# Kernel tuning notes

Measured on AMD Instinct MI355X. Metric: run time of the kernel, lower is better.

The kernel has to match this reference:

```python
import jax, jax.numpy as jnp
import numpy as np

EPS = 1e-12  # F.normalize eps
WIN_SIZE = 200
WIN_STEP = 30  # eval mode (training uses 10)
N_WIN = 30     # 31 windows from length-1100 axis, last one dropped


def setup_inputs() -> dict:
    key = jax.random.key(0)
    ks = jax.random.split(key, 6)
    dim, K, out_dim = 128, 64, 256
    N, H, W = 8, 16, 900
    s = 1.0 / np.sqrt(dim)
    return {
        "x": jax.random.normal(ks[0], (N, dim, H, W), dtype=jnp.float32),
        "cluster_centers": jax.random.uniform(ks[1], (K, dim), dtype=jnp.float32),
        "conv_w": jax.random.normal(ks[2], (K, dim), dtype=jnp.float32) * s,
        "conv_b": jax.random.normal(ks[3], (K,), dtype=jnp.float32) * s,
        "mlp_w": jax.random.normal(ks[4], (out_dim, K * dim), dtype=jnp.float32) * s,
        "mlp_b": jax.random.normal(ks[5], (out_dim,), dtype=jnp.float32) * s,
    }


def _l2norm(v, axis):
    return v / jnp.clip(jnp.linalg.norm(v, axis=axis, keepdims=True), EPS)


def reference(x, cluster_centers, conv_w, conv_b, mlp_w, mlp_b):
    N, C, H, W = x.shape
    K = conv_w.shape[0]
    # 1x1 conv -> soft assignment, softmax over clusters (dim=1 after view(N,K,HW))
    logits = jnp.einsum('nchw,kc->nkhw', x, conv_w) + conv_b[None, :, None, None]
    a = jax.nn.softmax(logits, axis=1)  # (N,K,H,W)
    # Fused weighted residual sum over H (torch sums dim=-2 of (N,K,C,H,W)):
    # vlad_pre[n,k,c,w] = sum_h a[n,k,h,w]*x[n,c,h,w] - centers[k,c]*sum_h a[n,k,h,w]
    wx = jnp.einsum('nkhw,nchw->nkcw', a, x)               # (N,K,C,W)
    asum = a.sum(axis=2)                                    # (N,K,W)
    res = wx - cluster_centers[None, :, :, None] * asum[:, :, None, :]
    # circular pad along yaw: [800:] ++ all ++ [:100] -> length 1100
    res = jnp.concatenate([res[..., 800:], res, res[..., :100]], axis=-1)
    # sliding-window sum, size 200 step 30, drop last window -> 30 windows
    cs = jnp.cumsum(res, axis=-1)
    cs = jnp.concatenate([jnp.zeros(res.shape[:-1] + (1,), res.dtype), cs], axis=-1)
    starts = jnp.arange(N_WIN) * WIN_STEP
    win = cs[..., starts + WIN_SIZE] - cs[..., starts]      # (N,K,C,30)
    vlad = jnp.transpose(win, (0, 3, 1, 2)).reshape(N * N_WIN, K, C)
    vlad = _l2norm(vlad, axis=2)                            # intra-norm per cluster
    vlad = _l2norm(vlad.reshape(N * N_WIN, K * C), axis=1)  # global norm
    out = vlad @ mlp_w.T + mlp_b
    out = _l2norm(out, axis=1)
    return out.reshape(N, N_WIN, -1)
```

## Files before the change

### kernel.cpp

```cpp
#include <hip/hip_runtime.h>
#include <cstddef>

#define EPSF 1e-12f
#define NCB 90
#define NT 30
#define ODIM 256
#define DDIM 8192

typedef unsigned short u16;
typedef __attribute__((ext_vector_type(8))) short short8;
typedef __attribute__((ext_vector_type(4))) float float4v;

__device__ inline u16 f2bf(float f) {
  union { float f; unsigned u; } v; v.f = f;
  unsigned r = v.u + 0x7FFFu + ((v.u >> 16) & 1u);
  return (u16)(r >> 16);
}
__device__ inline float bf2f(u16 h) {
  union { unsigned u; float f; } v; v.u = ((unsigned)h) << 16;
  return v.f;
}

__global__ __launch_bounds__(256, 2) void k1_assign(
    const float* __restrict__ x,
    const float* __restrict__ conv_w,
    const float* __restrict__ conv_b,
    float* __restrict__ P,
    float* __restrict__ PA)
{
  __shared__ u16 wfh[8192];
  __shared__ u16 wfl[8192];
  __shared__ u16 xtf[4096];
  __shared__ u16 xf[4096];
  __shared__ float As[64 * 33];
  __shared__ u16 afr[2048];
  __shared__ float Mf[32];
  __shared__ float sm4[128];
  __shared__ float pasum[256];

  const int bx = blockIdx.x;
  const int n = bx / NCB, cb = bx - n * NCB;
  const int t = threadIdx.x;
  const int lane = t & 63;
  const int w = t >> 6;

  const float* xn = x + (size_t)n * 1843200 + cb * 10;

#pragma unroll 4
  for (int i = 0; i < 32; ++i) {
    int e = t + 256 * i;
    int k = e >> 7, c = e & 127;
    float wv = conv_w[e];
    u16 h = f2bf(wv);
    float lo = wv - bf2f(h);
    int idx = (((k >> 4) * 4 + (c >> 5)) * 64 + (((c >> 3) & 3) << 4) + (k & 15)) * 8 + (c & 7);
    wfh[idx] = h;
    wfl[idx] = f2bf(lo);
  }

  const int colt = w & 1;
  const int kt0 = w >> 1;
  const float bk0 = conv_b[kt0 * 16 + (lane & 15)];
  const float bk1 = conv_b[(kt0 + 2) * 16 + (lane & 15)];

  float4v pacc[8];
#pragma unroll
  for (int i = 0; i < 8; ++i) pacc[i] = (float4v){0.f, 0.f, 0.f, 0.f};
  float pak = 0.f;

  for (int cc = 0; cc < 5; ++cc) {
    __syncthreads();
#pragma unroll
    for (int s = 0; s < 8; ++s) {
      int e2 = t + 256 * s;
      int c = e2 >> 4, p = e2 & 15;
      int cl = 2 * p;
      int g = cc * 32 + cl;
      int h = g / 10, wi = g - 10 * h;
      float2 val = *(const float2*)(xn + (size_t)c * 14400 + h * 900 + wi);
      u16 h0 = f2bf(val.x), h1 = f2bf(val.y);
      int ip = ((c >> 4) * 64 + ((cl >> 3) << 4) + (c & 15)) * 8 + (cl & 7);
      ushort2 pr; pr.x = h0; pr.y = h1;
      *(ushort2*)&xf[ip] = pr;
      int base_t = (((cl >> 4) * 4 + (c >> 5)) * 64 + (((c >> 3) & 3) << 4)) * 8 + (c & 7);
      xtf[base_t + ((cl & 15) << 3)] = h0;
      xtf[base_t + (((cl + 1) & 15) << 3)] = h1;
    }
    __syncthreads();

    {
      float4v d0 = (float4v){0.f, 0.f, 0.f, 0.f};
      float4v d1 = (float4v){0.f, 0.f, 0.f, 0.f};
#pragma unroll
      for (int cb32 = 0; cb32 < 4; ++cb32) {
        short8 xa = *(short8*)&xtf[((colt * 4 + cb32) * 64 + lane) * 8];
        short8 w0h = *(short8*)&wfh[((kt0 * 4 + cb32) * 64 + lane) * 8];
        short8 w0l = *(short8*)&wfl[((kt0 * 4 + cb32) * 64 + lane) * 8];
        short8 w1h = *(short8*)&wfh[(((kt0 + 2) * 4 + cb32) * 64 + lane) * 8];
        short8 w1l = *(short8*)&wfl[(((kt0 + 2) * 4 + cb32) * 64 + lane) * 8];
        d0 = __builtin_amdgcn_mfma_f32_16x16x32_bf16(xa, w0h, d0, 0, 0, 0);
        d0 = __builtin_amdgcn_mfma_f32_16x16x32_bf16(xa, w0l, d0, 0, 0, 0);
        d1 = __builtin_amdgcn_mfma_f32_16x16x32_bf16(xa, w1h, d1, 0, 0, 0);
        d1 = __builtin_amdgcn_mfma_f32_16x16x32_bf16(xa, w1l, d1, 0, 0, 0);
      }
      int colb = colt * 16 + ((lane >> 4) << 2);
      int kr0 = kt0 * 16 + (lane & 15);
      int kr1 = (kt0 + 2) * 16 + (lane & 15);
#pragma unroll
      for (int r = 0; r < 4; ++r) {
        As[kr0 * 33 + colb + r] = d0[r] + bk0;
        As[kr1 * 33 + colb + r] = d1[r] + bk1;
      }
    }
    __syncthreads();

    if (t < 32) {
      float m = -3.4e38f;
#pragma unroll
      for (int kk = 0; kk < 64; ++kk) m = fmaxf(m, As[kk * 33 + t]);
      Mf[t] = m;
    }
    __syncthreads();
    if (t < 128) {
      int col = t & 31, kg = t >> 5;
      float M = Mf[col], s = 0.f;
#pragma unroll
      for (int ii = 0; ii < 16; ++ii) {
        int a = (kg * 16 + ii) * 33 + col;
        float e = __expf(As[a] - M);
        As[a] = e;
        s += e;
      }
      sm4[kg * 32 + col] = s;
    }
    __syncthreads();

    {
      int k = t & 63, cg = t >> 6;
      union { u16 u[8]; short8 v; } cvt;
      float paks = 0.f;
#pragma unroll
      for (int j = 0; j < 8; ++j) {
        int col = cg * 8 + j;
        float inv = 1.f / (sm4[col] + sm4[32 + col] + sm4[64 + col] + sm4[96 + col]);
        float a = As[k * 33 + col] * inv;
        paks += a;
        cvt.u[j] = f2bf(a);
      }
      pak += paks;
      int dst = ((k >> 4) * 64 + (cg << 4) + (k & 15)) * 8;
      *(short8*)&afr[dst] = cvt.v;
    }
    __syncthreads();

    {
      short8 aa = *(short8*)&afr[(w * 64 + lane) * 8];
#pragma unroll
      for (int ct = 0; ct < 8; ++ct) {
        short8 xb = *(short8*)&xf[(ct * 64 + lane) * 8];
        pacc[ct] = __builtin_amdgcn_mfma_f32_16x16x32_bf16(aa, xb, pacc[ct], 0, 0, 0);
      }
    }
  }

  float* Pp = P + (size_t)(n * NCB + cb) * DDIM;
  {
    int krow = w * 16 + ((lane >> 4) << 2);
    int c0 = lane & 15;
#pragma unroll
    for (int ct = 0; ct < 8; ++ct)
#pragma unroll
      for (int r = 0; r < 4; ++r)
        Pp[(krow + r) * 128 + ct * 16 + c0] = pacc[ct][r];
  }
  pasum[t] = pak;
  __syncthreads();
  if (t < 64)
    PA[(size_t)(n * NCB + cb) * 64 + t] =
        pasum[t] + pasum[64 + t] + pasum[128 + t] + pasum[192 + t];
}

__global__ __launch_bounds__(256) void k2_vlad(
    const float* __restrict__ P, const float* __restrict__ PA,
    const float* __restrict__ centers, float* __restrict__ vlad,
    float* __restrict__ gss)
{
  __shared__ float Ak[16];
  __shared__ float red[4];
  const int b = blockIdx.x;
  const int win = b >> 2, eb = b & 3;
  const int n = win / NT, wt = win - n * NT;
  const int t = threadIdx.x;

  if (t < 64) {
    int kk = t >> 2, ii = t & 3;
    float s = 0.f;
#pragma unroll
    for (int ss = 0; ss < 5; ++ss) {
      int i = ii + 4 * ss;
      int cb = (3 * wt + 80 + i) % 90;
      s += PA[((size_t)n * NCB + cb) * 64 + eb * 16 + kk];
    }
    s += __shfl_xor(s, 1);
    s += __shfl_xor(s, 2);
    if (ii == 0) Ak[kk] = s;
  }
  __syncthreads();

  const int e0 = eb * 2048 + t * 8;
  float v[8];
#pragma unroll
  for (int j = 0; j < 8; ++j) v[j] = 0.f;
#pragma unroll 5
  for (int i = 0; i < 20; ++i) {
    int cb = (3 * wt + 80 + i) % 90;
    const float* Pp = P + ((size_t)n * NCB + cb) * DDIM + e0;
    float4 u0 = *(const float4*)Pp;
    float4 u1 = *(const float4*)(Pp + 4);
    v[0] += u0.x; v[1] += u0.y; v[2] += u0.z; v[3] += u0.w;
    v[4] += u1.x; v[5] += u1.y; v[6] += u1.z; v[7] += u1.w;
  }
  const float A = Ak[t >> 4];
  const float* ce = centers + e0;
  float ss8 = 0.f;
#pragma unroll
  for (int j = 0; j < 8; ++j) {
    float val = v[j] - ce[j] * A;
    v[j] = val;
    ss8 += val * val;
  }
  float ssg = ss8;
  ssg += __shfl_xor(ssg, 1);
  ssg += __shfl_xor(ssg, 2);
  ssg += __shfl_xor(ssg, 4);
  ssg += __shfl_xor(ssg, 8);
  float rn = 1.f / fmaxf(sqrtf(ssg), EPSF);
#pragma unroll
  for (int j = 0; j < 8; ++j) v[j] *= rn;
  float ts = ss8 * rn * rn;
  ts += __shfl_xor(ts, 1);
  ts += __shfl_xor(ts, 2);
  ts += __shfl_xor(ts, 4);
  ts += __shfl_xor(ts, 8);
  ts += __shfl_xor(ts, 16);
  ts += __shfl_xor(ts, 32);
  if ((t & 63) == 0) red[t >> 6] = ts;
  __syncthreads();
  if (t == 0) gss[(size_t)win * 4 + eb] = red[0] + red[1] + red[2] + red[3];

  float* vp = vlad + (size_t)win * DDIM + e0;
  *(float4*)vp = make_float4(v[0], v[1], v[2], v[3]);
  *(float4*)(vp + 4) = make_float4(v[4], v[5], v[6], v[7]);
}

__global__ __launch_bounds__(256) void k3_gemm(
    const float* __restrict__ vlad, const float* __restrict__ gss,
    const float* __restrict__ mlp_w, float* __restrict__ part)
{
  __shared__ float va[16 * 68];
  __shared__ float wbt[64 * 129];
  __shared__ float ga[16];
  const int bx = blockIdx.x;
  const int rt = bx % 15;
  const int hx = bx / 15;
  const int ot = hx & 1, ks = hx >> 1;
  const int t = threadIdx.x;

  if (t < 16) {
    int r = rt * 16 + t;
    float s = gss[r * 4] + gss[r * 4 + 1] + gss[r * 4 + 2] + gss[r * 4 + 3];
    ga[t] = 1.f / fmaxf(sqrtf(s), EPSF);
  }

  const int rr = (t >> 5) << 1;
  const int o0 = t & 31;
  float acc[2][4];
#pragma unroll
  for (int a = 0; a < 2; ++a)
#pragma unroll
    for (int u = 0; u < 4; ++u) acc[a][u] = 0.f;

  const int d0 = ks * 512;
  for (int dc = 0; dc < 512; dc += 64) {
    __syncthreads();
    {
      int r = t >> 4, dq = t & 15;
      float4 u = *(const float4*)(vlad + (size_t)(rt * 16 + r) * DDIM + d0 + dc + 4 * dq);
      float g = ga[r];
      u.x *= g; u.y *= g; u.z *= g; u.w *= g;
      *(float4*)&va[r * 68 + 4 * dq] = u;
    }
#pragma unroll
    for (int s = 0; s < 8; ++s) {
      int f = t + 256 * s;
      int o = f >> 4, dq = f & 15;
      float4 u = *(const float4*)(mlp_w + (size_t)(ot * 128 + o) * DDIM + d0 + dc + 4 * dq);
      wbt[(4 * dq + 0) * 129 + o] = u.x;
      wbt[(4 * dq + 1) * 129 + o] = u.y;
      wbt[(4 * dq + 2) * 129 + o] = u.z;
      wbt[(4 * dq + 3) * 129 + o] = u.w;
    }
    __syncthreads();
#pragma unroll 8
    for (int dd = 0; dd < 64; ++dd) {
      float x0 = va[rr * 68 + dd];
      float x1 = va[(rr + 1) * 68 + dd];
      float y0 = wbt[dd * 129 + o0];
      float y1 = wbt[dd * 129 + o0 + 32];
      float y2 = wbt[dd * 129 + o0 + 64];
      float y3 = wbt[dd * 129 + o0 + 96];
      acc[0][0] += x0 * y0; acc[0][1] += x0 * y1; acc[0][2] += x0 * y2; acc[0][3] += x0 * y3;
      acc[1][0] += x1 * y0; acc[1][1] += x1 * y1; acc[1][2] += x1 * y2; acc[1][3] += x1 * y3;
    }
  }
  float* pp = part + ((size_t)ks * 240 + rt * 16) * ODIM + ot * 128;
#pragma unroll
  for (int a = 0; a < 2; ++a)
#pragma unroll
    for (int u = 0; u < 4; ++u)
      pp[(rr + a) * ODIM + o0 + 32 * u] = acc[a][u];
}

__global__ __launch_bounds__(256) void k4_out(
    const float* __restrict__ part, const float* __restrict__ bias,
    float* __restrict__ out)
{
  __shared__ float red[4];
  const int r = blockIdx.x;
  const int o = threadIdx.x;
  float v = bias[o];
#pragma unroll
  for (int s = 0; s < 16; ++s) v += part[((size_t)s * 240 + r) * ODIM + o];
  float ss = v * v;
  ss += __shfl_xor(ss, 32);
  ss += __shfl_xor(ss, 16);
  ss += __shfl_xor(ss, 8);
  ss += __shfl_xor(ss, 4);
  ss += __shfl_xor(ss, 2);
  ss += __shfl_xor(ss, 1);
  if ((o & 63) == 0) red[o >> 6] = ss;
  __syncthreads();
  float total = red[0] + red[1] + red[2] + red[3];
  out[(size_t)r * ODIM + o] = v / fmaxf(sqrtf(total), EPSF);
}

extern "C" void kernel_launch(void* const* d_in, const int* in_sizes, int n_in,
                              void* d_out, int out_size, void* d_ws, size_t ws_size,
                              hipStream_t stream) {
  const float* x       = (const float*)d_in[0];
  const float* centers = (const float*)d_in[1];
  const float* conv_w  = (const float*)d_in[2];
  const float* conv_b  = (const float*)d_in[3];
  const float* mlp_w   = (const float*)d_in[4];
  const float* mlp_b   = (const float*)d_in[5];
  float* out = (float*)d_out;

  float* ws   = (float*)d_ws;
  float* P    = ws;
  float* PA   = P + (size_t)5898240;
  float* vlad = PA + (size_t)46080;
  float* gss  = vlad + (size_t)1966080;
  float* part = ws;

  k1_assign<<<dim3(8 * NCB), dim3(256), 0, stream>>>(x, conv_w, conv_b, P, PA);
  k2_vlad  <<<dim3(8 * NT * 4), dim3(256), 0, stream>>>(P, PA, centers, vlad, gss);
  k3_gemm  <<<dim3(480), dim3(256), 0, stream>>>(vlad, gss, mlp_w, part);
  k4_out   <<<dim3(240), dim3(256), 0, stream>>>(part, mlp_b, out);
}
```

Baseline: 187.1 us.

## Use bf16 MFMA for final GEMM, keep conv weights in registers, pad LDS

The final MLP GEMM moves from an fp32 LDS-tiled FMA loop to bf16 MFMA that reads operands directly from global memory. A new pre-kernel converts mlp_w to bf16, and the vlad kernel now writes bf16 output, which halves that traffic. In the assignment kernel the conv weight hi/lo split lives in registers instead of LDS, the x tiles get padded LDS layouts to reduce bank conflicts, and occupancy is raised to 3 blocks. The change lowers GEMM precision to plain bf16 and doubles the number of split-K partials summed in the output kernel.

After: 174.1 us. 1.07x faster.

```diff
diff --git a/kernel.cpp b/kernel.cpp
--- a/kernel.cpp
+++ b/kernel.cpp
@@ -21,17 +21,27 @@
   return v.f;
 }
 
-__global__ __launch_bounds__(256, 2) void k1_assign(
+__global__ __launch_bounds__(256) void k0_conv(
+    const float* __restrict__ w, u16* __restrict__ w16)
+{
+  int i = (blockIdx.x * 256 + threadIdx.x) * 8;
+  float4 a = *(const float4*)(w + i);
+  float4 b = *(const float4*)(w + i + 4);
+  union { u16 u[8]; short8 v; } o;
+  o.u[0] = f2bf(a.x); o.u[1] = f2bf(a.y); o.u[2] = f2bf(a.z); o.u[3] = f2bf(a.w);
+  o.u[4] = f2bf(b.x); o.u[5] = f2bf(b.y); o.u[6] = f2bf(b.z); o.u[7] = f2bf(b.w);
+  *(short8*)(w16 + i) = o.v;
+}
+
+__global__ __launch_bounds__(256, 3) void k1_assign(
     const float* __restrict__ x,
     const float* __restrict__ conv_w,
     const float* __restrict__ conv_b,
     float* __restrict__ P,
     float* __restrict__ PA)
 {
-  __shared__ u16 wfh[8192];
-  __shared__ u16 wfl[8192];
-  __shared__ u16 xtf[4096];
-  __shared__ u16 xf[4096];
+  __shared__ u16 xtf[4160];
+  __shared__ u16 xf[5120];
   __shared__ float As[64 * 33];
   __shared__ u16 afr[2048];
   __shared__ float Mf[32];
@@ -46,22 +56,39 @@
 
   const float* xn = x + (size_t)n * 1843200 + cb * 10;
 
-#pragma unroll 4
-  for (int i = 0; i < 32; ++i) {
-    int e = t + 256 * i;
-    int k = e >> 7, c = e & 127;
-    float wv = conv_w[e];
-    u16 h = f2bf(wv);
-    float lo = wv - bf2f(h);
-    int idx = (((k >> 4) * 4 + (c >> 5)) * 64 + (((c >> 3) & 3) << 4) + (k & 15)) * 8 + (c & 7);
-    wfh[idx] = h;
-    wfl[idx] = f2bf(lo);
-  }
-
   const int colt = w & 1;
   const int kt0 = w >> 1;
   const float bk0 = conv_b[kt0 * 16 + (lane & 15)];
   const float bk1 = conv_b[(kt0 + 2) * 16 + (lane & 15)];
+
+  short8 w0h[4], w0l[4], w1h[4], w1l[4];
+  {
+    int kr0 = kt0 * 16 + (lane & 15);
+    int kr1 = kr0 + 32;
+    int cbase = (lane >> 4) << 3;
+#pragma unroll
+    for (int cb32 = 0; cb32 < 4; ++cb32) {
+      const float* wp0 = conv_w + (size_t)kr0 * 128 + cb32 * 32 + cbase;
+      const float* wp1 = conv_w + (size_t)kr1 * 128 + cb32 * 32 + cbase;
+      union { u16 u[8]; short8 v; } hh, ll;
+#pragma unroll
+      for (int j = 0; j < 8; ++j) {
+        float fv = wp0[j];
+        u16 h = f2bf(fv);
+        hh.u[j] = h;
+        ll.u[j] = f2bf(fv - bf2f(h));
+      }
+      w0h[cb32] = hh.v; w0l[cb32] = ll.v;
+#pragma unroll
+      for (int j = 0; j < 8; ++j) {
+        float fv = wp1[j];
+        u16 h = f2bf(fv);
+        hh.u[j] = h;
+        ll.u[j] = f2bf(fv - bf2f(h));
+      }
+      w1h[cb32] = hh.v; w1l[cb32] = ll.v;
+    }
+  }
 
   float4v pacc[8];
 #pragma unroll
@@ -79,12 +106,14 @@
       int h = g / 10, wi = g - 10 * h;
       float2 val = *(const float2*)(xn + (size_t)c * 14400 + h * 900 + wi);
       u16 h0 = f2bf(val.x), h1 = f2bf(val.y);
-      int ip = ((c >> 4) * 64 + ((cl >> 3) << 4) + (c & 15)) * 8 + (cl & 7);
+      int ip = (c >> 4) * 640 + (p >> 2) * 160 + (c & 15) * 8 + (cl & 7);
       ushort2 pr; pr.x = h0; pr.y = h1;
       *(ushort2*)&xf[ip] = pr;
-      int base_t = (((cl >> 4) * 4 + (c >> 5)) * 64 + (((c >> 3) & 3) << 4)) * 8 + (c & 7);
-      xtf[base_t + ((cl & 15) << 3)] = h0;
-      xtf[base_t + (((cl + 1) & 15) << 3)] = h1;
+      int F = (p >> 3) * 4 + (c >> 5);
+      int L = (((c >> 3) & 3) << 4) + (cl & 15);
+      int i0 = F * 520 + L * 8 + (c & 7);
+      xtf[i0] = h0;
+      xtf[i0 + 8] = h1;
     }
     __syncthreads();
 
@@ -93,19 +122,15 @@
       float4v d1 = (float4v){0.f, 0.f, 0.f, 0.f};
 #pragma unroll
       for (int cb32 = 0; cb32 < 4; ++cb32) {
-        short8 xa = *(short8*)&xtf[((colt * 4 + cb32) * 64 + lane) * 8];
-        short8 w0h = *(short8*)&wfh[((kt0 * 4 + cb32) * 64 + lane) * 8];
-        short8 w0l = *(short8*)&wfl[((kt0 * 4 + cb32) * 64 + lane) * 8];
-        short8 w1h = *(short8*)&wfh[(((kt0 + 2) * 4 + cb32) * 64 + lane) * 8];
-        short8 w1l = *(short8*)&wfl[(((kt0 + 2) * 4 + cb32) * 64 + lane) * 8];
-        d0 = __builtin_amdgcn_mfma_f32_16x16x32_bf16(xa, w0h, d0, 0, 0, 0);
-        d0 = __builtin_amdgcn_mfma_f32_16x16x32_bf16(xa, w0l, d0, 0, 0, 0);
-        d1 = __builtin_amdgcn_mfma_f32_16x16x32_bf16(xa, w1h, d1, 0, 0, 0);
-        d1 = __builtin_amdgcn_mfma_f32_16x16x32_bf16(xa, w1l, d1, 0, 0, 0);
+        short8 xa = *(short8*)&xtf[(colt * 4 + cb32) * 520 + lane * 8];
+        d0 = __builtin_amdgcn_mfma_f32_16x16x32_bf16(xa, w0h[cb32], d0, 0, 0, 0);
+        d0 = __builtin_amdgcn_mfma_f32_16x16x32_bf16(xa, w0l[cb32], d0, 0, 0, 0);
+        d1 = __builtin_amdgcn_mfma_f32_16x16x32_bf16(xa, w1h[cb32], d1, 0, 0, 0);
+        d1 = __builtin_amdgcn_mfma_f32_16x16x32_bf16(xa, w1l[cb32], d1, 0, 0, 0);
       }
       int colb = colt * 16 + ((lane >> 4) << 2);
       int kr0 = kt0 * 16 + (lane & 15);
-      int kr1 = (kt0 + 2) * 16 + (lane & 15);
+      int kr1 = kr0 + 32;
 #pragma unroll
       for (int r = 0; r < 4; ++r) {
         As[kr0 * 33 + colb + r] = d0[r] + bk0;
@@ -157,7 +182,7 @@
       short8 aa = *(short8*)&afr[(w * 64 + lane) * 8];
 #pragma unroll
       for (int ct = 0; ct < 8; ++ct) {
-        short8 xb = *(short8*)&xf[(ct * 64 + lane) * 8];
+        short8 xb = *(short8*)&xf[ct * 640 + (lane >> 4) * 160 + (lane & 15) * 8];
         pacc[ct] = __builtin_amdgcn_mfma_f32_16x16x32_bf16(aa, xb, pacc[ct], 0, 0, 0);
       }
     }
@@ -182,7 +207,7 @@
 
 __global__ __launch_bounds__(256) void k2_vlad(
     const float* __restrict__ P, const float* __restrict__ PA,
-    const float* __restrict__ centers, float* __restrict__ vlad,
+    const float* __restrict__ centers, u16* __restrict__ vlad16,
     float* __restrict__ gss)
 {
   __shared__ float Ak[16];
@@ -235,8 +260,6 @@
   ssg += __shfl_xor(ssg, 4);
   ssg += __shfl_xor(ssg, 8);
   float rn = 1.f / fmaxf(sqrtf(ssg), EPSF);
-#pragma unroll
-  for (int j = 0; j < 8; ++j) v[j] *= rn;
   float ts = ss8 * rn * rn;
   ts += __shfl_xor(ts, 1);
   ts += __shfl_xor(ts, 2);
@@ -248,77 +271,62 @@
   __syncthreads();
   if (t == 0) gss[(size_t)win * 4 + eb] = red[0] + red[1] + red[2] + red[3];
 
-  float* vp = vlad + (size_t)win * DDIM + e0;
-  *(float4*)vp = make_float4(v[0], v[1], v[2], v[3]);
-  *(float4*)(vp + 4) = make_float4(v[4], v[5], v[6], v[7]);
+  union { u16 u[8]; short8 s; } o;
+#pragma unroll
+  for (int j = 0; j < 8; ++j) o.u[j] = f2bf(v[j] * rn);
+  *(short8*)(vlad16 + (size_t)win * DDIM + e0) = o.s;
 }
 
 __global__ __launch_bounds__(256) void k3_gemm(
-    const float* __restrict__ vlad, const float* __restrict__ gss,
-    const float* __restrict__ mlp_w, float* __restrict__ part)
-{
-  __shared__ float va[16 * 68];
-  __shared__ float wbt[64 * 129];
+    const u16* __restrict__ vlad16, const float* __restrict__ gss,
+    const u16* __restrict__ w16, float* __restrict__ part)
+{
   __shared__ float ga[16];
   const int bx = blockIdx.x;
   const int rt = bx % 15;
-  const int hx = bx / 15;
-  const int ot = hx & 1, ks = hx >> 1;
+  const int ks = bx / 15;
   const int t = threadIdx.x;
+  const int lane = t & 63;
+  const int w = t >> 6;
 
   if (t < 16) {
     int r = rt * 16 + t;
     float s = gss[r * 4] + gss[r * 4 + 1] + gss[r * 4 + 2] + gss[r * 4 + 3];
     ga[t] = 1.f / fmaxf(sqrtf(s), EPSF);
   }
-
-  const int rr = (t >> 5) << 1;
-  const int o0 = t & 31;
-  float acc[2][4];
-#pragma unroll
-  for (int a = 0; a < 2; ++a)
-#pragma unroll
-    for (int u = 0; u < 4; ++u) acc[a][u] = 0.f;
-
-  const int d0 = ks * 512;
-  for (int dc = 0; dc < 512; dc += 64) {
-    __syncthreads();
-    {
-      int r = t >> 4, dq = t & 15;
-      float4 u = *(const float4*)(vlad + (size_t)(rt * 16 + r) * DDIM + d0 + dc + 4 * dq);
-      float g = ga[r];
-      u.x *= g; u.y *= g; u.z *= g; u.w *= g;
-      *(float4*)&va[r * 68 + 4 * dq] = u;
-    }
-#pragma unroll
-    for (int s = 0; s < 8; ++s) {
-      int f = t + 256 * s;
-      int o = f >> 4, dq = f & 15;
-      float4 u = *(const float4*)(mlp_w + (size_t)(ot * 128 + o) * DDIM + d0 + dc + 4 * dq);
-      wbt[(4 * dq + 0) * 129 + o] = u.x;
-      wbt[(4 * dq + 1) * 129 + o] = u.y;
-      wbt[(4 * dq + 2) * 129 + o] = u.z;
-      wbt[(4 * dq + 3) * 129 + o] = u.w;
-    }
-    __syncthreads();
-#pragma unroll 8
-    for (int dd = 0; dd < 64; ++dd) {
-      float x0 = va[rr * 68 + dd];
-      float x1 = va[(rr + 1) * 68 + dd];
-      float y0 = wbt[dd * 129 + o0];
-      float y1 = wbt[dd * 129 + o0 + 32];
-      float y2 = wbt[dd * 129 + o0 + 64];
-      float y3 = wbt[dd * 129 + o0 + 96];
-      acc[0][0] += x0 * y0; acc[0][1] += x0 * y1; acc[0][2] += x0 * y2; acc[0][3] += x0 * y3;
-      acc[1][0] += x1 * y0; acc[1][1] += x1 * y1; acc[1][2] += x1 * y2; acc[1][3] += x1 * y3;
-    }
-  }
-  float* pp = part + ((size_t)ks * 240 + rt * 16) * ODIM + ot * 128;
-#pragma unroll
-  for (int a = 0; a < 2; ++a)
-#pragma unroll
-    for (int u = 0; u < 4; ++u)
-      pp[(rr + a) * ODIM + o0 + 32 * u] = acc[a][u];
+  __syncthreads();
+
+  const int m = lane & 15;
+  const int kg = lane >> 4;
+  const int d0 = ks * 256 + kg * 8;
+  const u16* arow = vlad16 + (size_t)(rt * 16 + m) * DDIM + d0;
+
+  float4v acc[4];
+#pragma unroll
+  for (int i = 0; i < 4; ++i) acc[i] = (float4v){0.f, 0.f, 0.f, 0.f};
+
+#pragma unroll
+  for (int ko = 0; ko < 8; ++ko) {
+    short8 a = *(const short8*)(arow + ko * 32);
+#pragma unroll
+    for (int nt = 0; nt < 4; ++nt) {
+      int o = w * 64 + nt * 16 + m;
+      short8 b = *(const short8*)(w16 + (size_t)o * DDIM + d0 + ko * 32);
+      acc[nt] = __builtin_amdgcn_mfma_f32_16x16x32_bf16(a, b, acc[nt], 0, 0, 0);
+    }
+  }
+
+  float g4[4];
+#pragma unroll
+  for (int r = 0; r < 4; ++r) g4[r] = ga[kg * 4 + r];
+  float* pp = part + ((size_t)ks * 240 + rt * 16) * ODIM;
+#pragma unroll
+  for (int nt = 0; nt < 4; ++nt) {
+    int o = w * 64 + nt * 16 + m;
+#pragma unroll
+    for (int r = 0; r < 4; ++r)
+      pp[(kg * 4 + r) * ODIM + o] = acc[nt][r] * g4[r];
+  }
 }
 
 __global__ __launch_bounds__(256) void k4_out(
@@ -330,7 +338,7 @@
   const int o = threadIdx.x;
   float v = bias[o];
 #pragma unroll
-  for (int s = 0; s < 16; ++s) v += part[((size_t)s * 240 + r) * ODIM + o];
+  for (int s = 0; s < 32; ++s) v += part[((size_t)s * 240 + r) * ODIM + o];
   float ss = v * v;
   ss += __shfl_xor(ss, 32);
   ss += __shfl_xor(ss, 16);
@@ -355,15 +363,17 @@
   const float* mlp_b   = (const float*)d_in[5];
   float* out = (float*)d_out;
 
-  float* ws   = (float*)d_ws;
-  float* P    = ws;
-  float* PA   = P + (size_t)5898240;
-  float* vlad = PA + (size_t)46080;
-  float* gss  = vlad + (size_t)1966080;
-  float* part = ws;
-
-  k1_assign<<<dim3(8 * NCB), dim3(256), 0, stream>>>(x, conv_w, conv_b, P, PA);
-  k2_vlad  <<<dim3(8 * NT * 4), dim3(256), 0, stream>>>(P, PA, centers, vlad, gss);
-  k3_gemm  <<<dim3(480), dim3(256), 0, stream>>>(vlad, gss, mlp_w, part);
-  k4_out   <<<dim3(240), dim3(256), 0, stream>>>(part, mlp_b, out);
-}
+  float* ws     = (float*)d_ws;
+  float* P      = ws;
+  float* PA     = ws + 5898240;
+  u16*   vlad16 = (u16*)(ws + 5944320);
+  float* gss    = (float*)((char*)d_ws + 27709440);
+  u16*   mlpw16 = (u16*)((char*)d_ws + 27713280);
+  float* part   = ws;
+
+  k0_conv  <<<dim3(1024),     dim3(256), 0, stream>>>(mlp_w, mlpw16);
+  k1_assign<<<dim3(8 * NCB),  dim3(256), 0, stream>>>(x, conv_w, conv_b, P, PA);
+  k2_vlad  <<<dim3(8 * NT * 4), dim3(256), 0, stream>>>(P, PA, centers, vlad16, gss);
+  k3_gemm  <<<dim3(480),      dim3(256), 0, stream>>>(vlad16, gss, mlpw16, part);
+  k4_out   <<<dim3(240),      dim3(256), 0, stream>>>(part, mlp_b, out);
+}
```
